# Kernel optimization log

Hardware: AMD Instinct MI355X
Metric: run time of the kernel (lower is better)

The kernel has to match this reference:

```python
import jax, jax.numpy as jnp
import numpy as np

CHUNK = 32
NH = 4
HID = 1024
DK = 128   # head_qk_dim
DV = 256   # head_v_dim
KD = 512   # key_dim
VD = 1024  # value_dim
LR = 32    # proj_low_rank_dim
GLR = 64   # gate_low_rank_dim
EPS = 1e-5


def setup_inputs() -> dict:
    key = jax.random.key(0)
    ks = jax.random.split(key, 16)
    def w(k, shape, scale=0.02):
        return jax.random.normal(k, shape, jnp.float32) * scale
    B, L = 2, 2048
    return {
        "hidden_states": jax.random.normal(ks[0], (B, L, HID), jnp.float32),
        "x0_mu": jax.random.uniform(ks[1], (HID,), jnp.float32),           # LerpLinear.mu
        "x0_w": w(ks[2], (5 * LR, HID)),                                   # x_proj[0].linear.weight
        "x2_w": w(ks[3], (HID, 5 * LR)),                                   # x_proj[2].weight
        "x_bias": w(ks[4], (5, HID)),
        "r_w": w(ks[5], (KD, HID)),
        "w_w1": w(ks[6], (GLR, HID)),                                      # w_proj LoRA down
        "w_w2": w(ks[7], (KD, GLR)),                                       # w_proj LoRA up
        "w_b2": w(ks[8], (KD,), 0.1),
        "k_w": w(ks[9], (KD, HID)),
        "v_w": w(ks[10], (VD, HID)),
        "g_w": w(ks[11], (VD, HID)),
        "bonus": w(ks[12], (NH, DK), 0.1),
        "gn_w": jnp.ones((VD,), jnp.float32),
        "gn_b": jnp.zeros((VD,), jnp.float32),
        "o_w": w(ks[13], (VD, HID)),
    }


def _chunk_rwkv6(q, k, v, w, u):
    """Faithful jax port of naive_chunk_rwkv6. q,k,w: [B,H,L,DK], v: [B,H,L,DV], u: [H,DK]."""
    B, H, L, D = q.shape
    n = L // CHUNK
    rs = lambda x: x.reshape(B, H, n, CHUNK, -1).astype(jnp.float32)
    q, k, v, w = rs(q), rs(k), rs(v), rs(w)
    wc = jnp.cumsum(w, axis=-2)                               # [B,H,n,c,DK]
    kw = k * jnp.exp(wc[..., -1:, :] - wc)
    wkv = jnp.einsum('bhncd,bhncp->bhndp', kw, v)             # per-chunk kv state update
    decay = jnp.exp(wc[:, :, :, -1, :])                        # [B,H,n,DK]

    def step(S, inp):
        d, kv = inp
        return S * d[..., None] + kv, S

    S0 = jnp.zeros((B, H, D, v.shape[-1]), jnp.float32)
    _, wkv_new = jax.lax.scan(step, S0,
                              (jnp.moveaxis(decay, 2, 0), jnp.moveaxis(wkv, 2, 0)))
    wkv_new = jnp.moveaxis(wkv_new, 0, 2)                      # state BEFORE each chunk

    qe = q * jnp.exp(wc - w)
    o_inter = jnp.einsum('bhndp,bhncd->bhncp', wkv_new, qe)

    # intra-chunk: A[i,j] = sum_d q_i k_j exp(wc_i - w_i - wc_j), j < i
    ke = k * jnp.exp(-wc)
    A = jnp.einsum('bhnid,bhnjd->bhnij', qe, ke)
    mask = jnp.tril(jnp.ones((CHUNK, CHUNK), bool), -1)
    A = jnp.where(mask, A, 0.0)
    o_intra = jnp.einsum('bhnij,bhnjp->bhnip', A, v)
    diag = jnp.einsum('bhncd,hd,bhncd->bhnc', q, u, k)         # bonus term (j == i)
    o_intra = o_intra + diag[..., None] * v
    return (o_inter + o_intra).reshape(B, H, L, -1)


def reference(hidden_states, x0_mu, x0_w, x2_w, x_bias, r_w, w_w1, w_w2, w_b2,
              k_w, v_w, g_w, bonus, gn_w, gn_b, o_w):
    x = hidden_states
    B, L, H = x.shape
    # time shift: shifted[t] = x[t-1], shifted[0] = 0
    shifted = jnp.pad(x, ((0, 0), (1, 0), (0, 0)))[:, :L]
    delta = shifted - x

    # x_proj: LerpLinear -> Tanh -> einsum with reshaped final Linear weight
    x5 = jnp.tanh((x + delta * x0_mu) @ x0_w.T).reshape(B, L, 5, LR)
    mix = jnp.einsum('blnr,hnr->blnh', x5, x2_w.reshape(H, 5, LR)) + x_bias  # [B,L,5,HID]
    r_mu, w_mu, k_mu, v_mu, g_mu = (mix[:, :, i, :] for i in range(5))

    r = (x + delta * r_mu) @ r_w.T
    wv = jnp.tanh((x + delta * w_mu) @ w_w1.T) @ w_w2.T + w_b2  # LoRA
    k = (x + delta * k_mu) @ k_w.T
    v = (x + delta * v_mu) @ v_w.T
    g = (x + delta * g_mu) @ g_w.T

    tohead = lambda t: t.reshape(B, L, NH, -1).transpose(0, 2, 1, 3)  # b l (h d) -> b h l d
    r_, w_, k_, v_ = tohead(r), tohead(wv), tohead(k), tohead(v)
    w_ = -jnp.exp(w_)

    o = _chunk_rwkv6(r_, k_, v_, w_, bonus)                    # [B,NH,L,DV]
    o = o.transpose(0, 2, 1, 3)                                # [B,L,NH,DV]

    # GroupNorm(num_groups=NH) over channels per token
    mean = o.mean(-1, keepdims=True)
    var = o.var(-1, keepdims=True)
    on = (o - mean) * jax.lax.rsqrt(var + EPS)
    on = on * gn_w.reshape(NH, DV) + gn_b.reshape(NH, DV)
    on = on.reshape(B, L, VD)

    out = on * (g * jax.nn.sigmoid(g))                          # swish gate
    return out @ o_w.T
```

## Files before the change

### kernel.cpp

```cpp
#include <hip/hip_runtime.h>


#define DEVI __device__ __forceinline__

namespace {

typedef unsigned short u16;
typedef unsigned int u32;
typedef __attribute__((ext_vector_type(8))) _Float16 f16x8;
typedef __attribute__((ext_vector_type(4))) float f32x4;

typedef __attribute__((address_space(1))) const u32 gu32;
typedef __attribute__((address_space(3))) u32 lu32;

constexpr int Lc = 2048;
constexpr int Tc = 4096;

constexpr size_t OFF_WKV   = 0;
constexpr size_t OFF_XM0   = 0;
constexpr size_t OFF_DELTA = 16777216;
constexpr size_t OFF_T160  = 33554432;
constexpr size_t OFF_XMW   = 36175872;
constexpr size_t OFF_X0WF  = 54001664;
constexpr size_t OFF_YWP   = 56623104;
constexpr size_t OFF_XMF   = 67108864;
constexpr size_t OFF_XM0F  = 67108864;
constexpr size_t OFF_WFIN  = 67108864;
constexpr size_t OFF_GATE  = 75497472;
constexpr size_t OFF_QE    = 100663296;
constexpr size_t OFF_OO    = 109051904;
constexpr size_t OFF_WF    = 125829120;
constexpr size_t OFF_DECAY = 132120576;
constexpr size_t OFF_OWB   = 136314880;
constexpr size_t OFF_RG    = 138412032;
constexpr size_t OFF_KG    = 146800640;
constexpr size_t OFF_VG    = 155189248;
constexpr size_t OFF_GG    = 171966464;
constexpr size_t WS_NEED   = 180355072;

DEVI float4 ld4(const float* p) { return *reinterpret_cast<const float4*>(p); }
DEVI void   st4(float* p, float4 v) { *reinterpret_cast<float4*>(p) = v; }
DEVI u16 f2h(float f) { _Float16 h = (_Float16)f; return *(u16*)&h; }
DEVI float h2f(u16 u) { _Float16 h = *(_Float16*)&u; return (float)h; }

DEVI void stage_swz(const u16* __restrict__ src, u16* __restrict__ dstBase,
                    int srow8, int k0, int lane) {
  const int rr = srow8 + (lane >> 3);
  const int ss = (lane & 7) ^ ((lane >> 3) & 7);
  __builtin_amdgcn_global_load_lds(
      (gu32*)(const void*)(src + (size_t)rr * 1024 + k0 + ss * 8),
      (lu32*)(void*)(dstBase + srow8 * 64), 16, 0, 0);
}
DEVI f16x8 read_swz(const u16* __restrict__ buf, int row, int slot_lin) {
  return *reinterpret_cast<const f16x8*>(buf + row * 64 + ((slot_lin ^ (row & 7)) * 8));
}

__global__ void kWA(const float* __restrict__ r_w, const float* __restrict__ k_w,
                    const float* __restrict__ v_w, const float* __restrict__ g_w,
                    const float* __restrict__ o_w, const float* __restrict__ x0_w,
                    const float* __restrict__ x, const float* __restrict__ x0_mu,
                    u16* __restrict__ Wf, u16* __restrict__ owb,
                    u16* __restrict__ x0wf, float* __restrict__ xm0,
                    float* __restrict__ delta, u16* __restrict__ xm0f) {
  if (blockIdx.x < 4256) {
    const size_t i = ((size_t)blockIdx.x * 256 + threadIdx.x) * 4;
    const float* src;
    u16* dst;
    if (i < 3145728) {
      src = (i < 524288)  ? r_w + i
          : (i < 1048576) ? k_w + (i - 524288)
          : (i < 2097152) ? v_w + (i - 1048576)
                          : g_w + (i - 2097152);
      dst = Wf + i;
    } else if (i < 4194304) {
      src = o_w + (i - 3145728);
      dst = owb + (i - 3145728);
    } else {
      src = x0_w + (i - 4194304);
      dst = x0wf + (i - 4194304);
    }
    float4 v = ld4(src);
    ushort4 h;
    h.x = f2h(v.x); h.y = f2h(v.y); h.z = f2h(v.z); h.w = f2h(v.w);
    *reinterpret_cast<ushort4*>(dst) = h;
  } else {
    const size_t i4 = (size_t)(blockIdx.x - 4256) * 256 + threadIdx.x;
    const int t = (int)(i4 >> 8);
    const int h4 = (int)(i4 & 255) * 4;
    float4 xv = ld4(x + (size_t)t * 1024 + h4);
    float4 xp = make_float4(0.f, 0.f, 0.f, 0.f);
    if (t & (Lc - 1)) xp = ld4(x + (size_t)(t - 1) * 1024 + h4);
    float4 mu = ld4(x0_mu + h4);
    float4 d;
    d.x = xp.x - xv.x; d.y = xp.y - xv.y; d.z = xp.z - xv.z; d.w = xp.w - xv.w;
    st4(delta + (size_t)t * 1024 + h4, d);
    float4 m0;
    m0.x = xv.x + d.x * mu.x; m0.y = xv.y + d.y * mu.y;
    m0.z = xv.z + d.z * mu.z; m0.w = xv.w + d.w * mu.w;
    st4(xm0 + (size_t)t * 1024 + h4, m0);
    ushort4 h;
    h.x = f2h(m0.x); h.y = f2h(m0.y); h.z = f2h(m0.z); h.w = f2h(m0.w);
    *reinterpret_cast<ushort4*>(xm0f + (size_t)t * 1024 + h4) = h;
  }
}

__global__ __launch_bounds__(256) void kA2f(
    const u16* __restrict__ xm0f, const u16* __restrict__ x0wf,
    float* __restrict__ t160) {
  __shared__ __align__(16) u16 sA[128 * 64];
  __shared__ __align__(16) u16 sB[128 * 64];
  const int mt = blockIdx.x, nt = blockIdx.y;
  const int ncols = nt ? 32 : 128;
  const int wcol0 = nt * 128;
  const u16* A = xm0f + (size_t)mt * 128 * 1024;
  const u16* B = x0wf + (size_t)wcol0 * 1024;
  const int tid = threadIdx.x;
  const int lane = tid & 63;
  const int wv = tid >> 6;
  const int wr = wv >> 1, wc = wv & 1;
  const int srow = wv * 32;
  f32x4 acc[4][4];
  #pragma unroll
  for (int i = 0; i < 4; ++i)
    #pragma unroll
    for (int j = 0; j < 4; ++j) acc[i][j] = {0.f, 0.f, 0.f, 0.f};

  for (int k0 = 0; k0 < 1024; k0 += 64) {
    #pragma unroll
    for (int c = 0; c < 4; ++c) {
      const int s8 = srow + c * 8;
      stage_swz(A, sA, s8, k0, lane);
      {
        const int rr = (s8 + (lane >> 3)) & (ncols - 1);
        const int ss = (lane & 7) ^ ((lane >> 3) & 7);
        __builtin_amdgcn_global_load_lds(
            (gu32*)(const void*)(B + (size_t)rr * 1024 + k0 + ss * 8),
            (lu32*)(void*)(sB + s8 * 64), 16, 0, 0);
      }
    }
    __syncthreads();
    #pragma unroll
    for (int kk = 0; kk < 2; ++kk) {
      const int sl = kk * 4 + (lane >> 4);
      f16x8 af[4], bf[4];
      #pragma unroll
      for (int m = 0; m < 4; ++m)
        af[m] = read_swz(sA, wr * 64 + m * 16 + (lane & 15), sl);
      #pragma unroll
      for (int j = 0; j < 4; ++j)
        bf[j] = read_swz(sB, wc * 64 + j * 16 + (lane & 15), sl);
      #pragma unroll
      for (int m = 0; m < 4; ++m)
        #pragma unroll
        for (int j = 0; j < 4; ++j)
          acc[m][j] = __builtin_amdgcn_mfma_f32_16x16x32_f16(af[m], bf[j], acc[m][j], 0, 0, 0);
    }
    __syncthreads();
  }
  #pragma unroll
  for (int m = 0; m < 4; ++m)
    #pragma unroll
    for (int r = 0; r < 4; ++r) {
      const int row = wr * 64 + m * 16 + (lane >> 4) * 4 + r;
      #pragma unroll
      for (int j = 0; j < 4; ++j) {
        const int col = wc * 64 + j * 16 + (lane & 15);
        if (col < ncols)
          t160[(size_t)(mt * 128 + row) * 160 + wcol0 + col] = tanhf(acc[m][j][r]);
      }
    }
}

__global__ __launch_bounds__(256) void kA2m5(
    const float* __restrict__ t160G, const float* __restrict__ x2_w,
    const float* __restrict__ x_bias, const float* __restrict__ xm0,
    const float* __restrict__ delta, const float* __restrict__ x0_mu,
    u16* __restrict__ xmf, float* __restrict__ xmw) {
  __shared__ float As[64 * 33];
  __shared__ float Ws[64 * 33];
  const int tid = threadIdx.x;
  const int n = blockIdx.x;
  const int m0 = blockIdx.y * 64, h0 = blockIdx.z * 64;
  const int rm = (tid >> 4) * 4, cn = (tid & 15) * 4;
  float4 xm4[4], dv4[4];
  #pragma unroll
  for (int i = 0; i < 4; ++i) {
    const size_t rowo = (size_t)(m0 + rm + i) * 1024 + h0 + cn;
    xm4[i] = ld4(xm0 + rowo);
    dv4[i] = ld4(delta + rowo);
  }
  const float4 mu4 = ld4(x0_mu + h0 + cn);
  const float4 b4 = ld4(x_bias + n * 1024 + h0 + cn);
  #pragma unroll
  for (int c = 0; c < 2; ++c) {
    int r = c * 32 + (tid >> 3);
    int col = (tid & 7) * 4;
    float4 a4 = ld4(t160G + (size_t)(m0 + r) * 160 + n * 32 + col);
    As[r * 33 + col + 0] = a4.x; As[r * 33 + col + 1] = a4.y;
    As[r * 33 + col + 2] = a4.z; As[r * 33 + col + 3] = a4.w;
    float4 w4 = ld4(x2_w + (size_t)(h0 + r) * 160 + n * 32 + col);
    Ws[r * 33 + col + 0] = w4.x; Ws[r * 33 + col + 1] = w4.y;
    Ws[r * 33 + col + 2] = w4.z; Ws[r * 33 + col + 3] = w4.w;
  }
  __syncthreads();
  float acc[4][4] = {};
  #pragma unroll
  for (int kk = 0; kk < 32; ++kk) {
    float a[4], w[4];
    #pragma unroll
    for (int i = 0; i < 4; ++i) a[i] = As[(rm + i) * 33 + kk];
    #pragma unroll
    for (int j = 0; j < 4; ++j) w[j] = Ws[(cn + j) * 33 + kk];
    #pragma unroll
    for (int i = 0; i < 4; ++i)
      #pragma unroll
      for (int j = 0; j < 4; ++j) acc[i][j] += a[i] * w[j];
  }
  const int pi = (n == 0) ? 0 : (n == 2) ? 1 : (n == 3) ? 2 : 3;
  #pragma unroll
  for (int i = 0; i < 4; ++i) {
    const size_t rowo = (size_t)(m0 + rm + i) * 1024 + h0 + cn;
    float4 o;
    o.x = xm4[i].x + dv4[i].x * (acc[i][0] + b4.x - mu4.x);
    o.y = xm4[i].y + dv4[i].y * (acc[i][1] + b4.y - mu4.y);
    o.z = xm4[i].z + dv4[i].z * (acc[i][2] + b4.z - mu4.z);
    o.w = xm4[i].w + dv4[i].w * (acc[i][3] + b4.w - mu4.w);
    if (n == 1) {
      st4(xmw + rowo, o);
    } else {
      ushort4 h;
      h.x = f2h(o.x); h.y = f2h(o.y); h.z = f2h(o.z); h.w = f2h(o.w);
      *reinterpret_cast<ushort4*>(xmf + (size_t)pi * Tc * 1024 + rowo) = h;
    }
  }
}

__global__ __launch_bounds__(256) void kWL(
    const float* __restrict__ xmw, const float* __restrict__ w_w1,
    float* __restrict__ ywp) {
  __shared__ float As[32 * 33];
  __shared__ float Ws[64 * 33];
  const int tid = threadIdx.x;
  const int t0 = blockIdx.x * 32;
  const int kbase = blockIdx.y * 256;
  const int rg = tid >> 5;
  const int cg = tid & 31;
  float acc[4][2] = {};
  for (int k0 = kbase; k0 < kbase + 256; k0 += 32) {
    __syncthreads();
    {
      int r = tid >> 3, c4 = (tid & 7) * 4;
      float4 a4 = ld4(xmw + (size_t)(t0 + r) * 1024 + k0 + c4);
      As[r * 33 + c4 + 0] = a4.x; As[r * 33 + c4 + 1] = a4.y;
      As[r * 33 + c4 + 2] = a4.z; As[r * 33 + c4 + 3] = a4.w;
    }
    #pragma unroll
    for (int c = 0; c < 2; ++c) {
      int r = c * 32 + (tid >> 3), c4 = (tid & 7) * 4;
      float4 w4 = ld4(w_w1 + (size_t)r * 1024 + k0 + c4);
      Ws[r * 33 + c4 + 0] = w4.x; Ws[r * 33 + c4 + 1] = w4.y;
      Ws[r * 33 + c4 + 2] = w4.z; Ws[r * 33 + c4 + 3] = w4.w;
    }
    __syncthreads();
    #pragma unroll
    for (int kk = 0; kk < 32; ++kk) {
      float a[4];
      #pragma unroll
      for (int i = 0; i < 4; ++i) a[i] = As[(rg * 4 + i) * 33 + kk];
      float w0 = Ws[cg * 33 + kk], w1 = Ws[(cg + 32) * 33 + kk];
      #pragma unroll
      for (int i = 0; i < 4; ++i) { acc[i][0] += a[i] * w0; acc[i][1] += a[i] * w1; }
    }
  }
  float* outp = ywp + (size_t)blockIdx.y * Tc * 64;
  #pragma unroll
  for (int i = 0; i < 4; ++i) {
    outp[(size_t)(t0 + rg * 4 + i) * 64 + cg]      = acc[i][0];
    outp[(size_t)(t0 + rg * 4 + i) * 64 + cg + 32] = acc[i][1];
  }
}

__global__ __launch_bounds__(256) void kB(
    const u16* __restrict__ xmf, const u16* __restrict__ Wf,
    u16* __restrict__ rG, u16* __restrict__ kG,
    u16* __restrict__ vG, u16* __restrict__ gG) {
  __shared__ __align__(16) u16 sA[128 * 64];
  __shared__ __align__(16) u16 sB[128 * 64];
  const int mt = blockIdx.x, nt = blockIdx.y;
  int plane, col0, ldc;
  u16* Ch;
  if (nt < 4)       { plane = 0; Ch = rG; ldc = 512;  col0 = nt * 128; }
  else if (nt < 8)  { plane = 1; Ch = kG; ldc = 512;  col0 = (nt - 4) * 128; }
  else if (nt < 16) { plane = 2; Ch = vG; ldc = 1024; col0 = (nt - 8) * 128; }
  else              { plane = 3; Ch = gG; ldc = 1024; col0 = (nt - 16) * 128; }
  const u16* A = xmf + ((size_t)plane * Tc + (size_t)mt * 128) * 1024;
  const u16* B = Wf + (size_t)nt * 128 * 1024;

  const int tid = threadIdx.x;
  const int lane = tid & 63;
  const int wv = tid >> 6;
  const int wr = wv >> 1, wc = wv & 1;
  const int srow = wv * 32;
  f32x4 acc[4][4];
  #pragma unroll
  for (int i = 0; i < 4; ++i)
    #pragma unroll
    for (int j = 0; j < 4; ++j) acc[i][j] = {0.f, 0.f, 0.f, 0.f};

  for (int k0 = 0; k0 < 1024; k0 += 64) {
    #pragma unroll
    for (int c = 0; c < 4; ++c) {
      const int s8 = srow + c * 8;
      stage_swz(A, sA, s8, k0, lane);
      stage_swz(B, sB, s8, k0, lane);
    }
    __syncthreads();
    #pragma unroll
    for (int kk = 0; kk < 2; ++kk) {
      const int sl = kk * 4 + (lane >> 4);
      f16x8 af[4], bf[4];
      #pragma unroll
      for (int m = 0; m < 4; ++m)
        af[m] = read_swz(sA, wr * 64 + m * 16 + (lane & 15), sl);
      #pragma unroll
      for (int j = 0; j < 4; ++j)
        bf[j] = read_swz(sB, wc * 64 + j * 16 + (lane & 15), sl);
      #pragma unroll
      for (int m = 0; m < 4; ++m)
        #pragma unroll
        for (int j = 0; j < 4; ++j)
          acc[m][j] = __builtin_amdgcn_mfma_f32_16x16x32_f16(af[m], bf[j], acc[m][j], 0, 0, 0);
    }
    __syncthreads();
  }
  #pragma unroll
  for (int m = 0; m < 4; ++m)
    #pragma unroll
    for (int r = 0; r < 4; ++r) {
      const int row = wr * 64 + m * 16 + (lane >> 4) * 4 + r;
      #pragma unroll
      for (int j = 0; j < 4; ++j) {
        const int col = wc * 64 + j * 16 + (lane & 15);
        Ch[(size_t)(mt * 128 + row) * ldc + col0 + col] = f2h(acc[m][j][r]);
      }
    }
}

__global__ __launch_bounds__(256) void kC(
    const float* __restrict__ ywp, const float* __restrict__ w_w2,
    const float* __restrict__ w_b2, float* __restrict__ wfin) {
  __shared__ float th[32 * 68];
  const int tid = threadIdx.x;
  const int t0 = blockIdx.x * 32;
  for (int idx = tid; idx < 32 * 64; idx += 256) {
    int i = idx >> 6, j = idx & 63;
    const size_t e = (size_t)(t0 + i) * 64 + j;
    float s = ywp[e] + ywp[(size_t)Tc * 64 + e] +
              ywp[(size_t)2 * Tc * 64 + e] + ywp[(size_t)3 * Tc * 64 + e];
    th[i * 68 + j] = tanhf(s);
  }
  __syncthreads();
  const int c = blockIdx.y * 256 + tid;
  float acc[32] = {};
  const float* w2 = w_w2 + (size_t)c * 64;
  for (int k = 0; k < 64; k += 4) {
    float4 wv = ld4(w2 + k);
    #pragma unroll
    for (int i = 0; i < 32; ++i) {
      float4 t4 = ld4(th + i * 68 + k);
      acc[i] += t4.x * wv.x + t4.y * wv.y + t4.z * wv.z + t4.w * wv.w;
    }
  }
  const float b = w_b2[c];
  #pragma unroll
  for (int i = 0; i < 32; ++i)
    wfin[(size_t)(t0 + i) * 512 + c] = -__expf(acc[i] + b);
}

__global__ __launch_bounds__(512) void kD1(
    const u16* __restrict__ rG, const u16* __restrict__ kG,
    const u16* __restrict__ vG, const float* __restrict__ wfin,
    const float* __restrict__ bonus, u16* __restrict__ wkvG,
    float* __restrict__ decayG, float* __restrict__ qeG, float* __restrict__ oG) {
  __shared__ __align__(16) float smem[13632];
  float* qeT   = smem;
  float* kwT   = smem + 4224;
  u16*   vl    = (u16*)(smem + 8448);
  float* wcl   = (float*)vl;
  float* Al    = smem + 8448 + 4096;
  float* diag2 = Al + 1024;
  const int tid = threadIdx.x;
  const int bid = blockIdx.x;
  const int nc = bid & 63, h = (bid >> 6) & 3, b = bid >> 8;
  const int tb = b * Lc + nc * 32;

  float4 wf[2];
  #pragma unroll
  for (int it = 0; it < 2; ++it) {
    int idx = it * 512 + tid;
    int c = idx >> 5, d4 = (idx & 31) * 4;
    wf[it] = ld4(wfin + (size_t)(tb + c) * 512 + h * 128 + d4);
  }
  ushort4 vreg[4];
  #pragma unroll
  for (int it = 0; it < 4; ++it) {
    int idx = it * 512 + tid;
    int c = idx >> 6, p4 = (idx & 63) * 4;
    vreg[it] = *reinterpret_cast<const ushort4*>(
        vG + (size_t)(tb + c) * 1024 + h * 256 + p4);
  }
  float rreg[8], kreg[8];
  #pragma unroll
  for (int it = 0; it < 8; ++it) {
    int idx = it * 512 + tid;
    int c = idx >> 7, d = idx & 127;
    rreg[it] = h2f(rG[(size_t)(tb + c) * 512 + h * 128 + d]);
    kreg[it] = h2f(kG[(size_t)(tb + c) * 512 + h * 128 + d]);
  }
  const float ureg = bonus[h * 128 + (tid & 127)];

  #pragma unroll
  for (int it = 0; it < 2; ++it) {
    int idx = it * 512 + tid;
    int c = idx >> 5, d4 = (idx & 31) * 4;
    st4(wcl + c * 128 + d4, wf[it]);
  }
  __syncthreads();
  if (tid < 128) {
    const int d = tid;
    float wv_[32];
    #pragma unroll
    for (int c = 0; c < 32; ++c) wv_[c] = wcl[c * 128 + d];
    float run = 0.f;
    #pragma unroll
    for (int c = 0; c < 32; ++c) { run += wv_[c]; wcl[c * 128 + d] = run; }
  }
  __syncthreads();
  #pragma unroll
  for (int it = 0; it < 8; ++it) {
    int idx = it * 512 + tid;
    int c = idx >> 7, d = idx & 127;
    int t = tb + c;
    float q = rreg[it];
    float k = kreg[it];
    float wcc = wcl[c * 128 + d];
    float wcp = (c > 0) ? wcl[(c - 1) * 128 + d] : 0.f;
    float wlast = wcl[31 * 128 + d];
    float qe = q * __expf(wcp);
    qeT[d * 33 + c] = q * __expf(wcp - wlast);
    kwT[d * 33 + c] = k * __expf(wlast - wcc);
    qeG[(size_t)t * 512 + h * 128 + d] = qe;
    if (c == 31) decayG[(size_t)bid * 128 + d] = __expf(wlast);
    float dv = q * k * ureg;
    #pragma unroll
    for (int m = 1; m < 64; m <<= 1) dv += __shfl_xor(dv, m, 64);
    if ((tid & 63) == 0) diag2[c * 2 + ((tid >> 6) & 1)] = dv;
  }
  __syncthreads();
  #pragma unroll
  for (int it = 0; it < 4; ++it) {
    int idx = it * 512 + tid;
    int c = idx >> 6, p4 = (idx & 63) * 4;
    *reinterpret_cast<ushort4*>(vl + c * 256 + p4) = vreg[it];
  }
  {
    const int j = tid & 31, i2 = tid >> 5;
    float a0 = 0.f, a1 = 0.f;
    for (int d = 0; d < 128; ++d) {
      float kv = kwT[d * 33 + j];
      a0 += qeT[d * 33 + i2] * kv;
      a1 += qeT[d * 33 + i2 + 16] * kv;
    }
    float dg0 = diag2[i2 * 2] + diag2[i2 * 2 + 1];
    float dg1 = diag2[(i2 + 16) * 2] + diag2[(i2 + 16) * 2 + 1];
    Al[i2 * 32 + j] = (j < i2) ? a0 : ((j == i2) ? dg0 : 0.f);
    Al[(i2 + 16) * 32 + j] = (j < i2 + 16) ? a1 : ((j == i2 + 16) ? dg1 : 0.f);
  }
  __syncthreads();
  const int pid = tid & 63, wvx = tid >> 6;
  const int p4 = pid * 4;
  {
    u16* wkvB = wkvG + (size_t)bid * (128 * 256);
    #pragma unroll
    for (int pp = 0; pp < 2; ++pp) {
      const int d0 = pp * 64 + wvx * 8;
      float4 acc[8];
      #pragma unroll
      for (int q = 0; q < 8; ++q) acc[q] = make_float4(0, 0, 0, 0);
      for (int c = 0; c < 32; ++c) {
        ushort4 v4u = *reinterpret_cast<const ushort4*>(vl + c * 256 + p4);
        float vx = h2f(v4u.x), vy = h2f(v4u.y), vz = h2f(v4u.z), vw = h2f(v4u.w);
        #pragma unroll
        for (int q = 0; q < 8; ++q) {
          float s = kwT[(d0 + q) * 33 + c];
          acc[q].x += vx * s; acc[q].y += vy * s;
          acc[q].z += vz * s; acc[q].w += vw * s;
        }
      }
      #pragma unroll
      for (int q = 0; q < 8; ++q) {
        ushort4 ob;
        ob.x = f2h(acc[q].x); ob.y = f2h(acc[q].y);
        ob.z = f2h(acc[q].z); ob.w = f2h(acc[q].w);
        *reinterpret_cast<ushort4*>(wkvB + (size_t)(d0 + q) * 256 + p4) = ob;
      }
    }
  }
  {
    float4 acc[4];
    #pragma unroll
    for (int q = 0; q < 4; ++q) acc[q] = make_float4(0, 0, 0, 0);
    for (int c = 0; c < 32; ++c) {
      ushort4 v4u = *reinterpret_cast<const ushort4*>(vl + c * 256 + p4);
      float vx = h2f(v4u.x), vy = h2f(v4u.y), vz = h2f(v4u.z), vw = h2f(v4u.w);
      #pragma unroll
      for (int q = 0; q < 4; ++q) {
        float a = Al[(wvx * 4 + q) * 32 + c];
        acc[q].x += vx * a; acc[q].y += vy * a;
        acc[q].z += vz * a; acc[q].w += vw * a;
      }
    }
    #pragma unroll
    for (int q = 0; q < 4; ++q)
      st4(oG + (size_t)(tb + wvx * 4 + q) * 1024 + h * 256 + p4, acc[q]);
  }
}

__global__ __launch_bounds__(256) void kD2(u16* __restrict__ wkvG,
                                           const float* __restrict__ decayG) {
  const int wvid = (blockIdx.x * 256 + threadIdx.x) >> 6;
  const int lane = threadIdx.x & 63;
  const int p4 = lane * 4;
  const int d = wvid & 127;
  const int bh = wvid >> 7;
  u16* base = wkvG + ((size_t)bh * 64 * 128 + d) * 256 + p4;
  const float* dbase = decayG + (size_t)bh * 64 * 128 + d;
  ushort4 kvb[4];
  float decb[4];
  #pragma unroll
  for (int i = 0; i < 4; ++i) {
    kvb[i] = *reinterpret_cast<const ushort4*>(base + (size_t)i * 32768);
    decb[i] = dbase[(size_t)i * 128];
  }
  float4 S = make_float4(0.f, 0.f, 0.f, 0.f);
  #pragma unroll
  for (int nc = 0; nc < 64; ++nc) {
    const int sl = nc & 3;
    ushort4 kv = kvb[sl];
    float dec = decb[sl];
    if (nc + 4 < 64) {
      kvb[sl] = *reinterpret_cast<const ushort4*>(base + (size_t)(nc + 4) * 32768);
      decb[sl] = dbase[(size_t)(nc + 4) * 128];
    }
    ushort4 ob;
    ob.x = f2h(S.x); ob.y = f2h(S.y); ob.z = f2h(S.z); ob.w = f2h(S.w);
    *reinterpret_cast<ushort4*>(base + (size_t)nc * 32768) = ob;
    S.x = S.x * dec + h2f(kv.x);
    S.y = S.y * dec + h2f(kv.y);
    S.z = S.z * dec + h2f(kv.z);
    S.w = S.w * dec + h2f(kv.w);
  }
}

__global__ __launch_bounds__(256) void kD3(
    const float* __restrict__ qeG, const u16* __restrict__ wkvG,
    const float* __restrict__ oG, const u16* __restrict__ gG,
    const float* __restrict__ gn_w, const float* __restrict__ gn_b,
    u16* __restrict__ gate) {
  __shared__ float qel[32 * 129];
  const int tid = threadIdx.x;
  const int bid = blockIdx.x;
  const int nc = bid & 63, h = (bid >> 6) & 3, b = bid >> 8;
  const int tb = b * Lc + nc * 32;
  for (int it = 0; it < 16; ++it) {
    int idx = it * 256 + tid;
    int c = idx >> 7, d = idx & 127;
    qel[c * 129 + d] = qeG[(size_t)(tb + c) * 512 + h * 128 + d];
  }
  __syncthreads();
  const int pid = tid & 63, wvx = tid >> 6;
  const int p4 = pid * 4;
  const int vd = h * 256 + p4;
  const float4 gw = ld4(gn_w + vd), gb = ld4(gn_b + vd);
  const u16* Sb = wkvG + (size_t)bid * (128 * 256);
  float4 acc[8];
  #pragma unroll
  for (int q = 0; q < 8; ++q) acc[q] = make_float4(0, 0, 0, 0);
  for (int d = 0; d < 128; ++d) {
    ushort4 s4 = *reinterpret_cast<const ushort4*>(Sb + (size_t)d * 256 + p4);
    float sx = h2f(s4.x), sy = h2f(s4.y), sz = h2f(s4.z), sw = h2f(s4.w);
    #pragma unroll
    for (int q = 0; q < 8; ++q) {
      float qv = qel[(wvx * 8 + q) * 129 + d];
      acc[q].x += sx * qv; acc[q].y += sy * qv;
      acc[q].z += sz * qv; acc[q].w += sw * qv;
    }
  }
  #pragma unroll
  for (int q = 0; q < 8; ++q) {
    const int t = tb + wvx * 8 + q;
    float4 cur = ld4(oG + (size_t)t * 1024 + vd);
    float4 o4;
    o4.x = cur.x + acc[q].x; o4.y = cur.y + acc[q].y;
    o4.z = cur.z + acc[q].z; o4.w = cur.w + acc[q].w;
    float s = o4.x + o4.y + o4.z + o4.w;
    float ss = o4.x * o4.x + o4.y * o4.y + o4.z * o4.z + o4.w * o4.w;
    #pragma unroll
    for (int m = 1; m < 64; m <<= 1) {
      s += __shfl_xor(s, m, 64);
      ss += __shfl_xor(ss, m, 64);
    }
    const float mean = s * (1.f / 256.f);
    const float var = ss * (1.f / 256.f) - mean * mean;
    const float rs = rsqrtf(var + 1e-5f);
    float4 on;
    on.x = (o4.x - mean) * rs * gw.x + gb.x;
    on.y = (o4.y - mean) * rs * gw.y + gb.y;
    on.z = (o4.z - mean) * rs * gw.z + gb.z;
    on.w = (o4.w - mean) * rs * gw.w + gb.w;
    ushort4 g4 = *reinterpret_cast<const ushort4*>(gG + (size_t)t * 1024 + vd);
    float gx = h2f(g4.x), gy = h2f(g4.y), gz = h2f(g4.z), gw_ = h2f(g4.w);
    float4 sw;
    sw.x = gx / (1.f + __expf(-gx));
    sw.y = gy / (1.f + __expf(-gy));
    sw.z = gz / (1.f + __expf(-gz));
    sw.w = gw_ / (1.f + __expf(-gw_));
    ushort4 ob;
    ob.x = f2h(on.x * sw.x); ob.y = f2h(on.y * sw.y);
    ob.z = f2h(on.z * sw.z); ob.w = f2h(on.w * sw.w);
    *reinterpret_cast<ushort4*>(gate + (size_t)t * 1024 + vd) = ob;
  }
}

__global__ __launch_bounds__(256) void kF(
    const u16* __restrict__ gate, const u16* __restrict__ owb,
    float* __restrict__ out) {
  __shared__ __align__(16) u16 Abuf[128 * 64];
  __shared__ __align__(16) u16 Bbuf[128 * 64];
  const int mt = blockIdx.x, nt = blockIdx.y;
  const u16* A = gate + (size_t)mt * 128 * 1024;
  const u16* W = owb + (size_t)nt * 128 * 1024;
  float* C = out + (size_t)mt * 128 * 1024 + nt * 128;
  const int tid = threadIdx.x;
  const int lane = tid & 63;
  const int wv = tid >> 6;
  const int wr = wv >> 1, wc = wv & 1;
  const int srow = wv * 32;
  f32x4 acc[4][4];
  #pragma unroll
  for (int i = 0; i < 4; ++i)
    #pragma unroll
    for (int j = 0; j < 4; ++j) acc[i][j] = {0.f, 0.f, 0.f, 0.f};
  for (int k0 = 0; k0 < 1024; k0 += 64) {
    #pragma unroll
    for (int c = 0; c < 4; ++c) {
      const int s8 = srow + c * 8;
      stage_swz(A, Abuf, s8, k0, lane);
      stage_swz(W, Bbuf, s8, k0, lane);
    }
    __syncthreads();
    #pragma unroll
    for (int kk = 0; kk < 2; ++kk) {
      const int sl = kk * 4 + (lane >> 4);
      f16x8 af[4], bf[4];
      #pragma unroll
      for (int m = 0; m < 4; ++m)
        af[m] = read_swz(Abuf, wr * 64 + m * 16 + (lane & 15), sl);
      #pragma unroll
      for (int j = 0; j < 4; ++j)
        bf[j] = read_swz(Bbuf, wc * 64 + j * 16 + (lane & 15), sl);
      #pragma unroll
      for (int m = 0; m < 4; ++m)
        #pragma unroll
        for (int j = 0; j < 4; ++j)
          acc[m][j] = __builtin_amdgcn_mfma_f32_16x16x32_f16(af[m], bf[j], acc[m][j], 0, 0, 0);
    }
    __syncthreads();
  }
  #pragma unroll
  for (int m = 0; m < 4; ++m)
    #pragma unroll
    for (int r = 0; r < 4; ++r) {
      const int row = wr * 64 + m * 16 + (lane >> 4) * 4 + r;
      #pragma unroll
      for (int j = 0; j < 4; ++j) {
        const int col = wc * 64 + j * 16 + (lane & 15);
        C[(size_t)row * 1024 + col] = acc[m][j][r];
      }
    }
}

}

extern "C" void kernel_launch(void* const* d_in, const int* in_sizes, int n_in,
                              void* d_out, int out_size, void* d_ws, size_t ws_size,
                              hipStream_t stream) {
  (void)in_sizes; (void)n_in; (void)out_size;
  if (ws_size < WS_NEED) return;

  const float* x      = (const float*)d_in[0];
  const float* x0_mu  = (const float*)d_in[1];
  const float* x0_w   = (const float*)d_in[2];
  const float* x2_w   = (const float*)d_in[3];
  const float* x_bias = (const float*)d_in[4];
  const float* r_w    = (const float*)d_in[5];
  const float* w_w1   = (const float*)d_in[6];
  const float* w_w2   = (const float*)d_in[7];
  const float* w_b2   = (const float*)d_in[8];
  const float* k_w    = (const float*)d_in[9];
  const float* v_w    = (const float*)d_in[10];
  const float* g_w    = (const float*)d_in[11];
  const float* bonus  = (const float*)d_in[12];
  const float* gn_w   = (const float*)d_in[13];
  const float* gn_b   = (const float*)d_in[14];
  const float* o_w    = (const float*)d_in[15];
  float* out = (float*)d_out;
  char* ws = (char*)d_ws;

  u16*   wkvG   = (u16*)(ws + OFF_WKV);
  float* xm0    = (float*)(ws + OFF_XM0);
  float* delta  = (float*)(ws + OFF_DELTA);
  float* t160   = (float*)(ws + OFF_T160);
  float* xmw    = (float*)(ws + OFF_XMW);
  u16*   x0wf   = (u16*)(ws + OFF_X0WF);
  float* ywp    = (float*)(ws + OFF_YWP);
  u16*   xm0f   = (u16*)(ws + OFF_XM0F);
  u16*   xmf    = (u16*)(ws + OFF_XMF);
  float* wfin   = (float*)(ws + OFF_WFIN);
  u16*   gate   = (u16*)(ws + OFF_GATE);
  float* qeG    = (float*)(ws + OFF_QE);
  float* oG     = (float*)(ws + OFF_OO);
  u16*   Wf     = (u16*)(ws + OFF_WF);
  float* decayG = (float*)(ws + OFF_DECAY);
  u16*   owb    = (u16*)(ws + OFF_OWB);
  u16*   rG     = (u16*)(ws + OFF_RG);
  u16*   kG     = (u16*)(ws + OFF_KG);
  u16*   vG     = (u16*)(ws + OFF_VG);
  u16*   gG     = (u16*)(ws + OFF_GG);

  kWA  <<<dim3(8352),        dim3(256), 0, stream>>>(r_w, k_w, v_w, g_w, o_w, x0_w,
                                                     x, x0_mu, Wf, owb, x0wf,
                                                     xm0, delta, xm0f);
  kA2f <<<dim3(32, 2),       dim3(256), 0, stream>>>(xm0f, x0wf, t160);
  kA2m5<<<dim3(5, 64, 16),   dim3(256), 0, stream>>>(t160, x2_w, x_bias, xm0, delta,
                                                     x0_mu, xmf, xmw);
  kWL  <<<dim3(128, 4),      dim3(256), 0, stream>>>(xmw, w_w1, ywp);
  kB   <<<dim3(32, 24),      dim3(256), 0, stream>>>(xmf, Wf, rG, kG, vG, gG);
  kC   <<<dim3(128, 2),      dim3(256), 0, stream>>>(ywp, w_w2, w_b2, wfin);
  kD1  <<<dim3(512),         dim3(512), 0, stream>>>(rG, kG, vG, wfin, bonus,
                                                     wkvG, decayG, qeG, oG);
  kD2  <<<dim3(256),         dim3(256), 0, stream>>>(wkvG, decayG);
  kD3  <<<dim3(512),         dim3(256), 0, stream>>>(qeG, wkvG, oG, gG,
                                                     gn_w, gn_b, gate);
  kF   <<<dim3(32, 8),       dim3(256), 0, stream>>>(gate, owb, out);
}
```

Before: 268.2 us.

## Recompute token-shift delta in kA2m5 and store qe/intra-chunk output as fp16

Stops materializing the fp32 delta and xm0 buffers in kWA. kA2m5 now recomputes them from x and the previous token. The intermediate qe and intra-chunk output o passed from kD1 to kD3 are stored as fp16 instead of fp32, halving that traffic. The goal is to cut global memory writes and reads between kernels. The cost is some precision loss on o and qe before the GroupNorm.

Result: slower. 288.2 us (+7.5%).

```diff
diff --git a/kernel.cpp b/kernel.cpp
--- a/kernel.cpp
+++ b/kernel.cpp
@@ -17,8 +17,6 @@
 constexpr int Tc = 4096;
 
 constexpr size_t OFF_WKV   = 0;
-constexpr size_t OFF_XM0   = 0;
-constexpr size_t OFF_DELTA = 16777216;
 constexpr size_t OFF_T160  = 33554432;
 constexpr size_t OFF_XMW   = 36175872;
 constexpr size_t OFF_X0WF  = 54001664;
@@ -60,8 +58,7 @@
                     const float* __restrict__ o_w, const float* __restrict__ x0_w,
                     const float* __restrict__ x, const float* __restrict__ x0_mu,
                     u16* __restrict__ Wf, u16* __restrict__ owb,
-                    u16* __restrict__ x0wf, float* __restrict__ xm0,
-                    float* __restrict__ delta, u16* __restrict__ xm0f) {
+                    u16* __restrict__ x0wf, u16* __restrict__ xm0f) {
   if (blockIdx.x < 4256) {
     const size_t i = ((size_t)blockIdx.x * 256 + threadIdx.x) * 4;
     const float* src;
@@ -91,13 +88,9 @@
     float4 xp = make_float4(0.f, 0.f, 0.f, 0.f);
     if (t & (Lc - 1)) xp = ld4(x + (size_t)(t - 1) * 1024 + h4);
     float4 mu = ld4(x0_mu + h4);
-    float4 d;
-    d.x = xp.x - xv.x; d.y = xp.y - xv.y; d.z = xp.z - xv.z; d.w = xp.w - xv.w;
-    st4(delta + (size_t)t * 1024 + h4, d);
     float4 m0;
-    m0.x = xv.x + d.x * mu.x; m0.y = xv.y + d.y * mu.y;
-    m0.z = xv.z + d.z * mu.z; m0.w = xv.w + d.w * mu.w;
-    st4(xm0 + (size_t)t * 1024 + h4, m0);
+    m0.x = xv.x + (xp.x - xv.x) * mu.x; m0.y = xv.y + (xp.y - xv.y) * mu.y;
+    m0.z = xv.z + (xp.z - xv.z) * mu.z; m0.w = xv.w + (xp.w - xv.w) * mu.w;
     ushort4 h;
     h.x = f2h(m0.x); h.y = f2h(m0.y); h.z = f2h(m0.z); h.w = f2h(m0.w);
     *reinterpret_cast<ushort4*>(xm0f + (size_t)t * 1024 + h4) = h;
@@ -173,8 +166,8 @@
 
 __global__ __launch_bounds__(256) void kA2m5(
     const float* __restrict__ t160G, const float* __restrict__ x2_w,
-    const float* __restrict__ x_bias, const float* __restrict__ xm0,
-    const float* __restrict__ delta, const float* __restrict__ x0_mu,
+    const float* __restrict__ x_bias, const float* __restrict__ x,
+    const float* __restrict__ x0_mu,
     u16* __restrict__ xmf, float* __restrict__ xmw) {
   __shared__ float As[64 * 33];
   __shared__ float Ws[64 * 33];
@@ -182,14 +175,20 @@
   const int n = blockIdx.x;
   const int m0 = blockIdx.y * 64, h0 = blockIdx.z * 64;
   const int rm = (tid >> 4) * 4, cn = (tid & 15) * 4;
+  const float4 mu4 = ld4(x0_mu + h0 + cn);
   float4 xm4[4], dv4[4];
   #pragma unroll
   for (int i = 0; i < 4; ++i) {
-    const size_t rowo = (size_t)(m0 + rm + i) * 1024 + h0 + cn;
-    xm4[i] = ld4(xm0 + rowo);
-    dv4[i] = ld4(delta + rowo);
-  }
-  const float4 mu4 = ld4(x0_mu + h0 + cn);
+    const int t = m0 + rm + i;
+    const size_t rowo = (size_t)t * 1024 + h0 + cn;
+    float4 xv = ld4(x + rowo);
+    float4 xp = make_float4(0.f, 0.f, 0.f, 0.f);
+    if (t & (Lc - 1)) xp = ld4(x + rowo - 1024);
+    dv4[i].x = xp.x - xv.x; dv4[i].y = xp.y - xv.y;
+    dv4[i].z = xp.z - xv.z; dv4[i].w = xp.w - xv.w;
+    xm4[i].x = xv.x + dv4[i].x * mu4.x; xm4[i].y = xv.y + dv4[i].y * mu4.y;
+    xm4[i].z = xv.z + dv4[i].z * mu4.z; xm4[i].w = xv.w + dv4[i].w * mu4.w;
+  }
   const float4 b4 = ld4(x_bias + n * 1024 + h0 + cn);
   #pragma unroll
   for (int c = 0; c < 2; ++c) {
@@ -381,7 +380,7 @@
     const u16* __restrict__ rG, const u16* __restrict__ kG,
     const u16* __restrict__ vG, const float* __restrict__ wfin,
     const float* __restrict__ bonus, u16* __restrict__ wkvG,
-    float* __restrict__ decayG, float* __restrict__ qeG, float* __restrict__ oG) {
+    float* __restrict__ decayG, u16* __restrict__ qeH, u16* __restrict__ oH) {
   __shared__ __align__(16) float smem[13632];
   float* qeT   = smem;
   float* kwT   = smem + 4224;
@@ -449,7 +448,7 @@
     float qe = q * __expf(wcp);
     qeT[d * 33 + c] = q * __expf(wcp - wlast);
     kwT[d * 33 + c] = k * __expf(wlast - wcc);
-    qeG[(size_t)t * 512 + h * 128 + d] = qe;
+    qeH[(size_t)t * 512 + h * 128 + d] = f2h(qe);
     if (c == 31) decayG[(size_t)bid * 128 + d] = __expf(wlast);
     float dv = q * k * ureg;
     #pragma unroll
@@ -521,8 +520,13 @@
       }
     }
     #pragma unroll
-    for (int q = 0; q < 4; ++q)
-      st4(oG + (size_t)(tb + wvx * 4 + q) * 1024 + h * 256 + p4, acc[q]);
+    for (int q = 0; q < 4; ++q) {
+      ushort4 ob;
+      ob.x = f2h(acc[q].x); ob.y = f2h(acc[q].y);
+      ob.z = f2h(acc[q].z); ob.w = f2h(acc[q].w);
+      *reinterpret_cast<ushort4*>(
+          oH + (size_t)(tb + wvx * 4 + q) * 1024 + h * 256 + p4) = ob;
+    }
   }
 }
 
@@ -563,8 +567,8 @@
 }
 
 __global__ __launch_bounds__(256) void kD3(
-    const float* __restrict__ qeG, const u16* __restrict__ wkvG,
-    const float* __restrict__ oG, const u16* __restrict__ gG,
+    const u16* __restrict__ qeH, const u16* __restrict__ wkvG,
+    const u16* __restrict__ oH, const u16* __restrict__ gG,
     const float* __restrict__ gn_w, const float* __restrict__ gn_b,
     u16* __restrict__ gate) {
   __shared__ float qel[32 * 129];
@@ -575,7 +579,7 @@
   for (int it = 0; it < 16; ++it) {
     int idx = it * 256 + tid;
     int c = idx >> 7, d = idx & 127;
-    qel[c * 129 + d] = qeG[(size_t)(tb + c) * 512 + h * 128 + d];
+    qel[c * 129 + d] = h2f(qeH[(size_t)(tb + c) * 512 + h * 128 + d]);
   }
   __syncthreads();
   const int pid = tid & 63, wvx = tid >> 6;
@@ -599,10 +603,10 @@
   #pragma unroll
   for (int q = 0; q < 8; ++q) {
     const int t = tb + wvx * 8 + q;
-    float4 cur = ld4(oG + (size_t)t * 1024 + vd);
+    ushort4 c4 = *reinterpret_cast<const ushort4*>(oH + (size_t)t * 1024 + vd);
     float4 o4;
-    o4.x = cur.x + acc[q].x; o4.y = cur.y + acc[q].y;
-    o4.z = cur.z + acc[q].z; o4.w = cur.w + acc[q].w;
+    o4.x = h2f(c4.x) + acc[q].x; o4.y = h2f(c4.y) + acc[q].y;
+    o4.z = h2f(c4.z) + acc[q].z; o4.w = h2f(c4.w) + acc[q].w;
     float s = o4.x + o4.y + o4.z + o4.w;
     float ss = o4.x * o4.x + o4.y * o4.y + o4.z * o4.z + o4.w * o4.w;
     #pragma unroll
@@ -718,8 +722,6 @@
   char* ws = (char*)d_ws;
 
   u16*   wkvG   = (u16*)(ws + OFF_WKV);
-  float* xm0    = (float*)(ws + OFF_XM0);
-  float* delta  = (float*)(ws + OFF_DELTA);
   float* t160   = (float*)(ws + OFF_T160);
   float* xmw    = (float*)(ws + OFF_XMW);
   u16*   x0wf   = (u16*)(ws + OFF_X0WF);
@@ -728,8 +730,8 @@
   u16*   xmf    = (u16*)(ws + OFF_XMF);
   float* wfin   = (float*)(ws + OFF_WFIN);
   u16*   gate   = (u16*)(ws + OFF_GATE);
-  float* qeG    = (float*)(ws + OFF_QE);
-  float* oG     = (float*)(ws + OFF_OO);
+  u16*   qeH    = (u16*)(ws + OFF_QE);
+  u16*   oH     = (u16*)(ws + OFF_OO);
   u16*   Wf     = (u16*)(ws + OFF_WF);
   float* decayG = (float*)(ws + OFF_DECAY);
   u16*   owb    = (u16*)(ws + OFF_OWB);
@@ -739,18 +741,17 @@
   u16*   gG     = (u16*)(ws + OFF_GG);
 
   kWA  <<<dim3(8352),        dim3(256), 0, stream>>>(r_w, k_w, v_w, g_w, o_w, x0_w,
-                                                     x, x0_mu, Wf, owb, x0wf,
-                                                     xm0, delta, xm0f);
+                                                     x, x0_mu, Wf, owb, x0wf, xm0f);
   kA2f <<<dim3(32, 2),       dim3(256), 0, stream>>>(xm0f, x0wf, t160);
-  kA2m5<<<dim3(5, 64, 16),   dim3(256), 0, stream>>>(t160, x2_w, x_bias, xm0, delta,
+  kA2m5<<<dim3(5, 64, 16),   dim3(256), 0, stream>>>(t160, x2_w, x_bias, x,
                                                      x0_mu, xmf, xmw);
   kWL  <<<dim3(128, 4),      dim3(256), 0, stream>>>(xmw, w_w1, ywp);
   kB   <<<dim3(32, 24),      dim3(256), 0, stream>>>(xmf, Wf, rG, kG, vG, gG);
   kC   <<<dim3(128, 2),      dim3(256), 0, stream>>>(ywp, w_w2, w_b2, wfin);
   kD1  <<<dim3(512),         dim3(512), 0, stream>>>(rG, kG, vG, wfin, bonus,
-                                                     wkvG, decayG, qeG, oG);
+                                                     wkvG, decayG, qeH, oH);
   kD2  <<<dim3(256),         dim3(256), 0, stream>>>(wkvG, decayG);
-  kD3  <<<dim3(512),         dim3(256), 0, stream>>>(qeG, wkvG, oG, gG,
+  kD3  <<<dim3(512),         dim3(256), 0, stream>>>(qeH, wkvG, oH, gG,
                                                      gn_w, gn_b, gate);
   kF   <<<dim3(32, 8),       dim3(256), 0, stream>>>(gate, owb, out);
 }
```
